# Performance work log

Hardware: AMD Instinct MI355X
Metric: run time of the kernel (lower is better)

The kernel has to match this reference:

```python
import jax, jax.numpy as jnp
import numpy as np
from jax import lax

B, T, C, H, HH, NL, O = 2048, 100, 8, 64, 128, 3, 10


def _linear_init(key, fan_in, fan_out):
    k1, k2 = jax.random.split(key)
    bound = 1.0 / np.sqrt(fan_in)
    W = jax.random.uniform(k1, (fan_in, fan_out), minval=-bound, maxval=bound, dtype=jnp.float32)
    b = jax.random.uniform(k2, (fan_out,), minval=-bound, maxval=bound, dtype=jnp.float32)
    return W, b


def setup_inputs() -> dict:
    key = jax.random.key(0)
    ks = jax.random.split(key, 8)
    coeffs = jax.random.normal(ks[0], (B, T, C), dtype=jnp.float32)
    y = jax.random.randint(ks[1], (B,), 0, O)
    times = jnp.linspace(0.0, 1.0, T, dtype=jnp.float32)
    W_init, b_init = _linear_init(ks[2], C, H)
    W_in, b_in = _linear_init(ks[3], H, HH)
    Wh_list, bh_list = [], []
    for i in range(NL - 1):
        W, b = _linear_init(jax.random.fold_in(ks[4], i), HH, HH)
        Wh_list.append(W)
        bh_list.append(b)
    W_h = jnp.stack(Wh_list)   # [NL-1, HH, HH]
    b_h = jnp.stack(bh_list)   # [NL-1, HH]
    W_out, b_out = _linear_init(ks[5], HH, H * C)
    W_read, b_read = _linear_init(ks[6], H, O)
    return {"coeffs": coeffs, "y": y, "times": times,
            "W_init": W_init, "b_init": b_init,
            "W_in": W_in, "b_in": b_in,
            "W_h": W_h, "b_h": b_h,
            "W_out": W_out, "b_out": b_out,
            "W_read": W_read, "b_read": b_read}


def _vector_field(z, W_in, b_in, W_h, b_h, W_out, b_out):
    # z: [B, H] -> f: [B, H, C] (linear -> relu -> ... -> linear -> tanh)
    h = jax.nn.relu(z @ W_in + b_in)
    for i in range(W_h.shape[0]):
        h = jax.nn.relu(h @ W_h[i] + b_h[i])
    f = jnp.tanh((h @ W_out + b_out).reshape(z.shape[0], H, C))
    return f


def reference(coeffs, y, times, W_init, b_init, W_in, b_in, W_h, b_h, W_out, b_out, W_read, b_read):
    # X(t) is linear interpolation of coeffs at `times`; dX/dt is piecewise
    # constant, so the CDE  dz = f(z) dX  is integrated with RK4 per grid
    # interval (the adaptive solver is replaced by a grid-aligned RK4 solve,
    # the standard deterministic reference for cdeint with linear control).
    z0 = coeffs[:, 0] @ W_init + b_init                    # X.evaluate(t0) = coeffs[:,0]
    dx = coeffs[:, 1:] - coeffs[:, :-1]                    # [B, T-1, C]
    dt = times[1:] - times[:-1]                            # [T-1]
    dxdt = dx / dt[None, :, None]                          # [B, T-1, C]

    def g(z, dxdt_i):
        f = _vector_field(z, W_in, b_in, W_h, b_h, W_out, b_out)   # [B,H,C]
        return jnp.einsum('bhc,bc->bh', f, dxdt_i)

    def step(z, xs):
        dxdt_i, dt_i = xs
        k1 = g(z, dxdt_i)
        k2 = g(z + 0.5 * dt_i * k1, dxdt_i)
        k3 = g(z + 0.5 * dt_i * k2, dxdt_i)
        k4 = g(z + dt_i * k3, dxdt_i)
        z_new = z + (dt_i / 6.0) * (k1 + 2.0 * k2 + 2.0 * k3 + k4)
        return z_new, None

    zT, _ = lax.scan(step, z0, (jnp.swapaxes(dxdt, 0, 1), dt))
    logits = zT @ W_read + b_read                          # [B, O]
    logp = jax.nn.log_softmax(logits, axis=-1)
    loss = -jnp.take_along_axis(logp, y[:, None], axis=1).mean()
    accuracy = (jnp.argmax(logits, axis=1) == y).sum().astype(logits.dtype)
    return loss, accuracy
```

## Files before the change

kernel.cpp:

```cpp
#include <hip/hip_runtime.h>

#define BB    2048
#define TT    100
#define CC    8
#define HD    64
#define HHD   128
#define OO    10
#define MROWS 8
#define NTHR  512

__device__ __forceinline__ float fast_tanh(float x) {
  float e = __expf(2.0f * x);
  return 1.0f - 2.0f / (e + 1.0f);
}

__global__ void zero_out_k(float* o) {
  if (threadIdx.x < 2) o[threadIdx.x] = 0.0f;
}

__device__ __forceinline__ void hidden_layer(const float* __restrict__ Wg,
                                             const float (*pin)[HHD],
                                             float (*pout)[HHD],
                                             int l, int kb, int rb) {
  float a0[4] = {0.f,0.f,0.f,0.f};
  float a1[4] = {0.f,0.f,0.f,0.f};
#pragma unroll
  for (int h = 0; h < 2; ++h) {
    float wx[16], wy[16];
#pragma unroll
    for (int j = 0; j < 16; ++j) {
      const float* wr = Wg + (kb + 16*h + j) * HHD;
      wx[j] = wr[l];
      wy[j] = wr[l + 64];
    }
#pragma unroll
    for (int rr = 0; rr < 4; ++rr) {
      const float* pr = &pin[rb + rr][kb + 16*h];
      const float4 h0 = *(const float4*)(pr);
      const float4 h1 = *(const float4*)(pr + 4);
      const float4 h2 = *(const float4*)(pr + 8);
      const float4 h3 = *(const float4*)(pr + 12);
      const float hk[16] = {
        fmaxf(h0.x,0.f), fmaxf(h0.y,0.f), fmaxf(h0.z,0.f), fmaxf(h0.w,0.f),
        fmaxf(h1.x,0.f), fmaxf(h1.y,0.f), fmaxf(h1.z,0.f), fmaxf(h1.w,0.f),
        fmaxf(h2.x,0.f), fmaxf(h2.y,0.f), fmaxf(h2.z,0.f), fmaxf(h2.w,0.f),
        fmaxf(h3.x,0.f), fmaxf(h3.y,0.f), fmaxf(h3.z,0.f), fmaxf(h3.w,0.f) };
#pragma unroll
      for (int k = 0; k < 16; ++k) {
        a0[rr] = fmaf(hk[k], wx[k], a0[rr]);
        a1[rr] = fmaf(hk[k], wy[k], a1[rr]);
      }
    }
  }
#pragma unroll
  for (int rr = 0; rr < 4; ++rr) {
    atomicAdd(&pout[rb + rr][l],      a0[rr]);
    atomicAdd(&pout[rb + rr][l + 64], a1[rr]);
  }
}

__global__ void __launch_bounds__(NTHR)
cde_main(const float* __restrict__ coeffs, const int* __restrict__ yy,
         const float* __restrict__ times,
         const float* __restrict__ W_init, const float* __restrict__ b_init,
         const float* __restrict__ W_in,  const float* __restrict__ b_in,
         const float* __restrict__ W_h,   const float* __restrict__ b_h,
         const float* __restrict__ W_out, const float* __restrict__ b_out,
         const float* __restrict__ W_read,const float* __restrict__ b_read,
         float* __restrict__ out)
{
  __shared__ float sZs[MROWS][HD];
  __shared__ float pA [MROWS][HHD];
  __shared__ float p1 [MROWS][HHD];
  __shared__ float p2 [MROWS][HHD];
  __shared__ float pB [MROWS][576];
  __shared__ float sDx[MROWS][CC];
  __shared__ float sLog[MROWS][OO];

  const int t    = threadIdx.x;
  const int wv   = t >> 6;
  const int l    = t & 63;
  const int row0 = blockIdx.x * MROWS;
  const int q    = wv & 3;
  const int rb   = 4 * (wv >> 2);
  const int colb = 256 * (wv >> 2) + 4 * l;

  const float binx = b_in[l],      biny = b_in[l + 64];
  const float b1x  = b_h[l],       b1y  = b_h[l + 64];
  const float b2x  = b_h[HHD + l], b2y  = b_h[HHD + l + 64];
  const float boutv = b_out[t];

  float z0, kacc = 0.f;
  {
    const float* cf = coeffs + (size_t)(row0 + wv) * (TT*CC);
    float a = b_init[l];
#pragma unroll
    for (int c = 0; c < CC; ++c) a = fmaf(cf[c], W_init[c*HD + l], a);
    z0 = a;
    sZs[wv][l] = a;
  }

  pA[wv][l] = binx;  pA[wv][l + 64] = biny;
  p1[wv][l] = b1x;   p1[wv][l + 64] = b1y;
  p2[wv][l] = b2x;   p2[wv][l + 64] = b2y;
#pragma unroll
  for (int r = 0; r < MROWS; ++r) pB[r][t + (t >> 3)] = boutv;
  __syncthreads();

#pragma unroll 1
  for (int step = 0; step < TT-1; ++step) {
    const float dti = times[step+1] - times[step];
    if (t < 64) {
      const int r = t >> 3, c = t & 7;
      const float* cf = coeffs + (size_t)(row0 + r)*(TT*CC) + step*CC + c;
      sDx[r][c] = (cf[CC] - cf[0]) / dti;
    }

#pragma unroll 1
    for (int s = 0; s < 4; ++s) {
      {
        const int kb = 16 * q;
        float wx[16], wy[16];
#pragma unroll
        for (int j = 0; j < 16; ++j) {
          const float* wr = W_in + (kb + j) * HHD;
          wx[j] = wr[l];
          wy[j] = wr[l + 64];
        }
#pragma unroll
        for (int rr = 0; rr < 4; ++rr) {
          const float* zr = &sZs[rb + rr][kb];
          const float4 za = *(const float4*)(zr);
          const float4 zb = *(const float4*)(zr + 4);
          const float4 zc = *(const float4*)(zr + 8);
          const float4 zd = *(const float4*)(zr + 12);
          const float zk[16] = {za.x, za.y, za.z, za.w, zb.x, zb.y, zb.z, zb.w,
                                zc.x, zc.y, zc.z, zc.w, zd.x, zd.y, zd.z, zd.w};
          float a0 = 0.f, a1 = 0.f;
#pragma unroll
          for (int k = 0; k < 16; ++k) {
            a0 = fmaf(zk[k], wx[k], a0);
            a1 = fmaf(zk[k], wy[k], a1);
          }
          atomicAdd(&pA[rb + rr][l],      a0);
          atomicAdd(&pA[rb + rr][l + 64], a1);
        }
#pragma unroll
        for (int r = 0; r < MROWS; ++r) pB[r][t + (t >> 3)] = boutv;
      }
      __syncthreads();
      hidden_layer(W_h, pA, p1, l, 32*q, rb);
      __syncthreads();
      hidden_layer(W_h + HHD*HHD, p1, p2, l, 32*q, rb);
      pA[wv][l] = binx;  pA[wv][l + 64] = biny;
      __syncthreads();
      {
        float acc[MROWS][4];
#pragma unroll
        for (int r = 0; r < MROWS; ++r)
#pragma unroll
          for (int c = 0; c < 4; ++c) acc[r][c] = 0.f;

        const float* wp = W_out + (size_t)(32*q) * (HD*CC) + colb;
#pragma unroll
        for (int kc = 0; kc < 8; ++kc) {
          float4 w4[4];
#pragma unroll
          for (int j = 0; j < 4; ++j)
            w4[j] = *(const float4*)(wp + (4*kc + j)*(HD*CC));
          const int k0 = 32*q + 4*kc;
#pragma unroll
          for (int r = 0; r < MROWS; ++r) {
            const float4 hv = *(const float4*)&p2[r][k0];
            const float hf[4] = { fmaxf(hv.x,0.f), fmaxf(hv.y,0.f),
                                  fmaxf(hv.z,0.f), fmaxf(hv.w,0.f) };
#pragma unroll
            for (int j = 0; j < 4; ++j) {
              acc[r][0] = fmaf(hf[j], w4[j].x, acc[r][0]);
              acc[r][1] = fmaf(hf[j], w4[j].y, acc[r][1]);
              acc[r][2] = fmaf(hf[j], w4[j].z, acc[r][2]);
              acc[r][3] = fmaf(hf[j], w4[j].w, acc[r][3]);
            }
          }
        }
#pragma unroll
        for (int r = 0; r < MROWS; ++r)
#pragma unroll
          for (int c = 0; c < 4; ++c) {
            const int col = colb + c;
            atomicAdd(&pB[r][col + (col >> 3)], acc[r][c]);
          }
        p1[wv][l] = b1x;  p1[wv][l + 64] = b1y;
      }
      __syncthreads();
      {
        const float* pr = &pB[wv][9*l];
        const float u0 = pr[0], u1 = pr[1], u2 = pr[2], u3 = pr[3];
        const float u4 = pr[4], u5 = pr[5], u6 = pr[6], u7 = pr[7];
        const float4 d0 = *(const float4*)&sDx[wv][0];
        const float4 d1 = *(const float4*)&sDx[wv][4];
        float g = fast_tanh(u0)*d0.x + fast_tanh(u1)*d0.y
                + fast_tanh(u2)*d0.z + fast_tanh(u3)*d0.w
                + fast_tanh(u4)*d1.x + fast_tanh(u5)*d1.y
                + fast_tanh(u6)*d1.z + fast_tanh(u7)*d1.w;
        if (s == 0)      kacc = g;
        else if (s == 3) kacc += g;
        else             kacc += 2.0f * g;
        float zs;
        if (s == 3) {
          z0 = z0 + dti * (1.0f/6.0f) * kacc;
          zs = z0;
        } else {
          zs = z0 + ((s == 2) ? dti : 0.5f * dti) * g;
        }
        sZs[wv][l] = zs;
        p2[wv][l] = b2x;  p2[wv][l + 64] = b2y;
      }
      __syncthreads();
    }
  }

  if (t < MROWS * OO) {
    const int r = t / OO, o = t % OO;
    float a = b_read[o];
#pragma unroll 8
    for (int k = 0; k < HD; ++k) a = fmaf(sZs[r][k], W_read[k*OO + o], a);
    sLog[r][o] = a;
  }
  __syncthreads();
  if (t < 64) {
    float lv = 0.f, cv = 0.f;
    if (t < MROWS) {
      const int r = t;
      float mx = sLog[r][0]; int am = 0;
#pragma unroll
      for (int o = 1; o < OO; ++o) { const float v = sLog[r][o]; if (v > mx) { mx = v; am = o; } }
      float se = 0.f;
#pragma unroll
      for (int o = 0; o < OO; ++o) se += expf(sLog[r][o] - mx);
      const float lse = mx + logf(se);
      const int yr = yy[row0 + r];
      lv = (lse - sLog[r][yr]) * (1.0f / (float)BB);
      cv = (am == yr) ? 1.0f : 0.0f;
    }
    lv += __shfl_xor(lv, 1); lv += __shfl_xor(lv, 2); lv += __shfl_xor(lv, 4);
    cv += __shfl_xor(cv, 1); cv += __shfl_xor(cv, 2); cv += __shfl_xor(cv, 4);
    if (t == 0) { atomicAdd(&out[0], lv); atomicAdd(&out[1], cv); }
  }
}

extern "C" void kernel_launch(void* const* d_in, const int* in_sizes, int n_in,
                              void* d_out, int out_size, void* d_ws, size_t ws_size,
                              hipStream_t stream) {
  const float* coeffs = (const float*)d_in[0];
  const int*   y      = (const int*)  d_in[1];
  const float* times  = (const float*)d_in[2];
  const float* W_init = (const float*)d_in[3];
  const float* b_init = (const float*)d_in[4];
  const float* W_in   = (const float*)d_in[5];
  const float* b_in   = (const float*)d_in[6];
  const float* W_h    = (const float*)d_in[7];
  const float* b_h    = (const float*)d_in[8];
  const float* W_out  = (const float*)d_in[9];
  const float* b_out  = (const float*)d_in[10];
  const float* W_read = (const float*)d_in[11];
  const float* b_read = (const float*)d_in[12];
  float* out = (float*)d_out;

  zero_out_k<<<1, 64, 0, stream>>>(out);
  cde_main<<<BB/MROWS, NTHR, 0, stream>>>(coeffs, y, times, W_init, b_init,
                                          W_in, b_in, W_h, b_h, W_out, b_out,
                                          W_read, b_read, out);
}
```

Baseline: 18.57 ms.

## Halve rows per block and repartition K across all eight waves

Each block now handles 4 batch rows instead of 8, which doubles the grid to 512 blocks. Inside a block, the input and hidden layers split the reduction dimension across all 8 waves, each covering all rows, instead of 4 K-slices times 2 row groups. Launch bounds ask for 4 blocks per CU to improve occupancy and latency hiding in this latency-bound sequential RK4 loop. In exchange, each block reloads the same weights for half as many rows, and the shared-memory atomics and per-step barrier work are amortized over fewer rows.

```diff
diff --git a/kernel.cpp b/kernel.cpp
--- a/kernel.cpp
+++ b/kernel.cpp
@@ -6,7 +6,7 @@
 #define HD    64
 #define HHD   128
 #define OO    10
-#define MROWS 8
+#define MROWS 4
 #define NTHR  512
 
 __device__ __forceinline__ float fast_tanh(float x) {
@@ -21,45 +21,43 @@
 __device__ __forceinline__ void hidden_layer(const float* __restrict__ Wg,
                                              const float (*pin)[HHD],
                                              float (*pout)[HHD],
-                                             int l, int kb, int rb) {
-  float a0[4] = {0.f,0.f,0.f,0.f};
-  float a1[4] = {0.f,0.f,0.f,0.f};
-#pragma unroll
-  for (int h = 0; h < 2; ++h) {
-    float wx[16], wy[16];
-#pragma unroll
-    for (int j = 0; j < 16; ++j) {
-      const float* wr = Wg + (kb + 16*h + j) * HHD;
-      wx[j] = wr[l];
-      wy[j] = wr[l + 64];
-    }
-#pragma unroll
-    for (int rr = 0; rr < 4; ++rr) {
-      const float* pr = &pin[rb + rr][kb + 16*h];
-      const float4 h0 = *(const float4*)(pr);
-      const float4 h1 = *(const float4*)(pr + 4);
-      const float4 h2 = *(const float4*)(pr + 8);
-      const float4 h3 = *(const float4*)(pr + 12);
-      const float hk[16] = {
-        fmaxf(h0.x,0.f), fmaxf(h0.y,0.f), fmaxf(h0.z,0.f), fmaxf(h0.w,0.f),
-        fmaxf(h1.x,0.f), fmaxf(h1.y,0.f), fmaxf(h1.z,0.f), fmaxf(h1.w,0.f),
-        fmaxf(h2.x,0.f), fmaxf(h2.y,0.f), fmaxf(h2.z,0.f), fmaxf(h2.w,0.f),
-        fmaxf(h3.x,0.f), fmaxf(h3.y,0.f), fmaxf(h3.z,0.f), fmaxf(h3.w,0.f) };
-#pragma unroll
-      for (int k = 0; k < 16; ++k) {
-        a0[rr] = fmaf(hk[k], wx[k], a0[rr]);
-        a1[rr] = fmaf(hk[k], wy[k], a1[rr]);
-      }
-    }
-  }
-#pragma unroll
-  for (int rr = 0; rr < 4; ++rr) {
-    atomicAdd(&pout[rb + rr][l],      a0[rr]);
-    atomicAdd(&pout[rb + rr][l + 64], a1[rr]);
-  }
-}
-
-__global__ void __launch_bounds__(NTHR)
+                                             int l, int kb) {
+  float wx[16], wy[16];
+#pragma unroll
+  for (int j = 0; j < 16; ++j) {
+    const float* wr = Wg + (kb + j) * HHD;
+    wx[j] = wr[l];
+    wy[j] = wr[l + 64];
+  }
+  float a0[MROWS], a1[MROWS];
+#pragma unroll
+  for (int rr = 0; rr < MROWS; ++rr) { a0[rr] = 0.f; a1[rr] = 0.f; }
+#pragma unroll
+  for (int rr = 0; rr < MROWS; ++rr) {
+    const float* pr = &pin[rr][kb];
+    const float4 h0 = *(const float4*)(pr);
+    const float4 h1 = *(const float4*)(pr + 4);
+    const float4 h2 = *(const float4*)(pr + 8);
+    const float4 h3 = *(const float4*)(pr + 12);
+    const float hk[16] = {
+      fmaxf(h0.x,0.f), fmaxf(h0.y,0.f), fmaxf(h0.z,0.f), fmaxf(h0.w,0.f),
+      fmaxf(h1.x,0.f), fmaxf(h1.y,0.f), fmaxf(h1.z,0.f), fmaxf(h1.w,0.f),
+      fmaxf(h2.x,0.f), fmaxf(h2.y,0.f), fmaxf(h2.z,0.f), fmaxf(h2.w,0.f),
+      fmaxf(h3.x,0.f), fmaxf(h3.y,0.f), fmaxf(h3.z,0.f), fmaxf(h3.w,0.f) };
+#pragma unroll
+    for (int k = 0; k < 16; ++k) {
+      a0[rr] = fmaf(hk[k], wx[k], a0[rr]);
+      a1[rr] = fmaf(hk[k], wy[k], a1[rr]);
+    }
+  }
+#pragma unroll
+  for (int rr = 0; rr < MROWS; ++rr) {
+    atomicAdd(&pout[rr][l],      a0[rr]);
+    atomicAdd(&pout[rr][l + 64], a1[rr]);
+  }
+}
+
+__global__ void __launch_bounds__(NTHR, 4)
 cde_main(const float* __restrict__ coeffs, const int* __restrict__ yy,
          const float* __restrict__ times,
          const float* __restrict__ W_init, const float* __restrict__ b_init,
@@ -82,7 +80,6 @@
   const int l    = t & 63;
   const int row0 = blockIdx.x * MROWS;
   const int q    = wv & 3;
-  const int rb   = 4 * (wv >> 2);
   const int colb = 256 * (wv >> 2) + 4 * l;
 
   const float binx = b_in[l],      biny = b_in[l + 64];
@@ -90,19 +87,18 @@
   const float b2x  = b_h[HHD + l], b2y  = b_h[HHD + l + 64];
   const float boutv = b_out[t];
 
-  float z0, kacc = 0.f;
-  {
+  float z0 = 0.f, kacc = 0.f;
+  if (wv < MROWS) {
     const float* cf = coeffs + (size_t)(row0 + wv) * (TT*CC);
     float a = b_init[l];
 #pragma unroll
     for (int c = 0; c < CC; ++c) a = fmaf(cf[c], W_init[c*HD + l], a);
     z0 = a;
     sZs[wv][l] = a;
-  }
-
-  pA[wv][l] = binx;  pA[wv][l + 64] = biny;
-  p1[wv][l] = b1x;   p1[wv][l + 64] = b1y;
-  p2[wv][l] = b2x;   p2[wv][l + 64] = b2y;
+    pA[wv][l] = binx;  pA[wv][l + 64] = biny;
+    p1[wv][l] = b1x;   p1[wv][l + 64] = b1y;
+    p2[wv][l] = b2x;   p2[wv][l + 64] = b2y;
+  }
 #pragma unroll
   for (int r = 0; r < MROWS; ++r) pB[r][t + (t >> 3)] = boutv;
   __syncthreads();
@@ -110,7 +106,7 @@
 #pragma unroll 1
   for (int step = 0; step < TT-1; ++step) {
     const float dti = times[step+1] - times[step];
-    if (t < 64) {
+    if (t < MROWS * CC) {
       const int r = t >> 3, c = t & 7;
       const float* cf = coeffs + (size_t)(row0 + r)*(TT*CC) + step*CC + c;
       sDx[r][c] = (cf[CC] - cf[0]) / dti;
@@ -119,40 +115,37 @@
 #pragma unroll 1
     for (int s = 0; s < 4; ++s) {
       {
-        const int kb = 16 * q;
-        float wx[16], wy[16];
-#pragma unroll
-        for (int j = 0; j < 16; ++j) {
+        const int kb = 8 * wv;
+        float wx[8], wy[8];
+#pragma unroll
+        for (int j = 0; j < 8; ++j) {
           const float* wr = W_in + (kb + j) * HHD;
           wx[j] = wr[l];
           wy[j] = wr[l + 64];
         }
 #pragma unroll
-        for (int rr = 0; rr < 4; ++rr) {
-          const float* zr = &sZs[rb + rr][kb];
+        for (int rr = 0; rr < MROWS; ++rr) {
+          const float* zr = &sZs[rr][kb];
           const float4 za = *(const float4*)(zr);
           const float4 zb = *(const float4*)(zr + 4);
-          const float4 zc = *(const float4*)(zr + 8);
-          const float4 zd = *(const float4*)(zr + 12);
-          const float zk[16] = {za.x, za.y, za.z, za.w, zb.x, zb.y, zb.z, zb.w,
-                                zc.x, zc.y, zc.z, zc.w, zd.x, zd.y, zd.z, zd.w};
+          const float zk[8] = {za.x, za.y, za.z, za.w, zb.x, zb.y, zb.z, zb.w};
           float a0 = 0.f, a1 = 0.f;
 #pragma unroll
-          for (int k = 0; k < 16; ++k) {
+          for (int k = 0; k < 8; ++k) {
             a0 = fmaf(zk[k], wx[k], a0);
             a1 = fmaf(zk[k], wy[k], a1);
           }
-          atomicAdd(&pA[rb + rr][l],      a0);
-          atomicAdd(&pA[rb + rr][l + 64], a1);
+          atomicAdd(&pA[rr][l],      a0);
+          atomicAdd(&pA[rr][l + 64], a1);
         }
 #pragma unroll
         for (int r = 0; r < MROWS; ++r) pB[r][t + (t >> 3)] = boutv;
       }
       __syncthreads();
-      hidden_layer(W_h, pA, p1, l, 32*q, rb);
-      __syncthreads();
-      hidden_layer(W_h + HHD*HHD, p1, p2, l, 32*q, rb);
-      pA[wv][l] = binx;  pA[wv][l + 64] = biny;
+      hidden_layer(W_h, pA, p1, l, 16 * wv);
+      __syncthreads();
+      hidden_layer(W_h + HHD*HHD, p1, p2, l, 16 * wv);
+      if (wv < MROWS) { pA[wv][l] = binx;  pA[wv][l + 64] = biny; }
       __syncthreads();
       {
         float acc[MROWS][4];
@@ -190,10 +183,10 @@
             const int col = colb + c;
             atomicAdd(&pB[r][col + (col >> 3)], acc[r][c]);
           }
-        p1[wv][l] = b1x;  p1[wv][l + 64] = b1y;
+        if (wv < MROWS) { p1[wv][l] = b1x;  p1[wv][l + 64] = b1y; }
       }
       __syncthreads();
-      {
+      if (wv < MROWS) {
         const float* pr = &pB[wv][9*l];
         const float u0 = pr[0], u1 = pr[1], u2 = pr[2], u3 = pr[3];
         const float u4 = pr[4], u5 = pr[5], u6 = pr[6], u7 = pr[7];
@@ -243,8 +236,8 @@
       lv = (lse - sLog[r][yr]) * (1.0f / (float)BB);
       cv = (am == yr) ? 1.0f : 0.0f;
     }
-    lv += __shfl_xor(lv, 1); lv += __shfl_xor(lv, 2); lv += __shfl_xor(lv, 4);
-    cv += __shfl_xor(cv, 1); cv += __shfl_xor(cv, 2); cv += __shfl_xor(cv, 4);
+    lv += __shfl_xor(lv, 1); lv += __shfl_xor(lv, 2);
+    cv += __shfl_xor(cv, 1); cv += __shfl_xor(cv, 2);
     if (t == 0) { atomicAdd(&out[0], lv); atomicAdd(&out[1], cv); }
   }
 }
```

New measurement: 25.12 ms. 1.35x slower.
